# Kernel tuning notes

Hardware: AMD Instinct MI355X
Metric: run time of the kernel (lower is better)

Reference implementation:

```python
import jax, jax.numpy as jnp
import numpy as np


def setup_inputs() -> dict:
    key = jax.random.key(0)
    k1, k2, k3, k4 = jax.random.split(key, 4)
    B, S, D = 2, 2048, 1024
    return {
        "X": jax.random.normal(k1, (B, S, D), dtype=jnp.float32),
        "W_q": jax.random.normal(k2, (D, D), dtype=jnp.float32),
        "W_k": jax.random.normal(k3, (D, D), dtype=jnp.float32),
        "W_v": jax.random.normal(k4, (D, D), dtype=jnp.float32),
        "n_heads": 16,
    }


def reference(X, W_q, W_k, W_v, n_heads):
    B, S, D = X.shape
    H = n_heads
    dh = D // H
    # QKV projections, split heads: [B,S,D] -> [H,B,S,dh]
    def split_heads(Y):
        return Y.reshape(B, S, H, dh).transpose(2, 0, 1, 3)
    Q = split_heads(X @ W_q)
    K = split_heads(X @ W_k)
    V = split_heads(X @ W_v)
    scale = 1.0 / jnp.sqrt(jnp.asarray(dh, dtype=X.dtype))
    # [H,B,S,S] attention scores (naive, matches the original)
    scores = jax.nn.softmax(jnp.einsum("hbqd,hbkd->hbqk", Q, K) * scale, axis=-1)
    out = jnp.einsum("hbqk,hbkd->hbqd", scores, V)  # [H,B,S,dh]
    # torch.concat(out, 0) over leading H dim -> [H*B, S, dh]
    return out.reshape(H * B, S, dh)
```

## Files before the change

### kernel.cpp

```cpp
#include <hip/hip_runtime.h>

typedef unsigned short u16;
typedef unsigned int u32;
typedef __bf16 bf16x8 __attribute__((ext_vector_type(8)));
typedef float f32x4 __attribute__((ext_vector_type(4)));
typedef float f32x16 __attribute__((ext_vector_type(16)));

extern "C" __device__ float __ocml_native_exp2_f32(float);

#define WT_HI_E  ((size_t)0)
#define WT_LO_E  ((size_t)3 << 20)
#define Q_HI_E   ((size_t)14 << 20)
#define Q_LO_E   ((size_t)18 << 20)
#define K_HI_E   ((size_t)22 << 20)
#define K_LO_E   ((size_t)26 << 20)
#define V_HI_E   ((size_t)30 << 20)

__device__ __forceinline__ u16 bf16_rne(float x) {
  u32 u = __float_as_uint(x);
  u32 r = (u + 0x7fffu + ((u >> 16) & 1u)) >> 16;
  return (u16)r;
}
__device__ __forceinline__ float bf16_f(u16 h) {
  return __uint_as_float(((u32)h) << 16);
}
__device__ __forceinline__ u16 f2bf(float x) {
  __bf16 b = (__bf16)x;
  return __builtin_bit_cast(u16, b);
}

__device__ __forceinline__ void gload16(const u16* g, u16* l) {
  __builtin_amdgcn_global_load_lds(
      (const __attribute__((address_space(1))) void*)g,
      (__attribute__((address_space(3))) void*)l, 16, 0, 0);
}

__global__ __launch_bounds__(256) void k_split(const float* __restrict__ w0,
                                               const float* __restrict__ w1,
                                               const float* __restrict__ w2,
                                               u16* __restrict__ ws) {
  int wb = blockIdx.x;
  int z = wb >> 8;
  int rem = wb & 255;
  int by = (rem >> 4) * 64, bx = (rem & 15) * 64;
  const float* W = (z == 0) ? w0 : ((z == 1) ? w1 : w2);
  u16* th = ws + WT_HI_E + (size_t)z * (1u << 20);
  u16* tl = ws + WT_LO_E + (size_t)z * (1u << 20);
  __shared__ float tile[64][65];
  int tx = threadIdx.x & 15, ty = threadIdx.x >> 4;
#pragma unroll
  for (int i = 0; i < 4; i++) {
    int r = ty + i * 16;
    float4 v = *(const float4*)(W + (size_t)(by + r) * 1024 + bx + tx * 4);
    tile[r][tx * 4 + 0] = v.x;
    tile[r][tx * 4 + 1] = v.y;
    tile[r][tx * 4 + 2] = v.z;
    tile[r][tx * 4 + 3] = v.w;
  }
  __syncthreads();
#pragma unroll
  for (int p = 0; p < 2; p++) {
    int t = threadIdx.x + 256 * p;
    int kc = t & 7, nl = t >> 3;
    u32 Hh[4], Ll[4];
#pragma unroll
    for (int u = 0; u < 4; u++) {
      float v0 = tile[kc * 8 + 2 * u][nl];
      float v1 = tile[kc * 8 + 2 * u + 1][nl];
      u16 h0 = f2bf(v0);
      u16 h1 = f2bf(v1);
      u16 l0 = f2bf(v0 - bf16_f(h0));
      u16 l1 = f2bf(v1 - bf16_f(h1));
      Hh[u] = (u32)h0 | ((u32)h1 << 16);
      Ll[u] = (u32)l0 | ((u32)l1 << 16);
    }
    size_t o = (size_t)(bx + nl) * 1024 + by + kc * 8;
    *(uint4*)(th + o) = make_uint4(Hh[0], Hh[1], Hh[2], Hh[3]);
    *(uint4*)(tl + o) = make_uint4(Ll[0], Ll[1], Ll[2], Ll[3]);
  }
}

__global__ __launch_bounds__(256, 4) void k_proj(const float* __restrict__ X,
                                                 u16* __restrict__ ws) {
  int id = blockIdx.x;
  int xcd = id & 7;
  int loc = id >> 3;
  int m_loc = loc & 7;
  int rest = loc >> 3;
  int n_blk = rest & 7, z = rest >> 3;
  int M0 = (xcd * 8 + m_loc) * 64;
  int N0 = n_blk * 128;

  const u16* Wh = ws + WT_HI_E + (size_t)z * (1u << 20);
  const u16* Wl = ws + WT_LO_E + (size_t)z * (1u << 20);
  u16* dsth = ws + ((z == 0) ? Q_HI_E : ((z == 1) ? K_HI_E : V_HI_E));
  u16* dstl = (z == 0) ? (ws + Q_LO_E) : ((z == 1) ? (ws + K_LO_E) : (u16*)0);

  __shared__ u16 smem[12288];
  float* sXf = (float*)smem;
  u16* sWh = smem + 4096;
  u16* sWl = smem + 8192;

  int tid = threadIdx.x, lane = tid & 63, w = tid >> 6;
  int quad = lane >> 4, l16 = lane & 15;
  int mb = (w & 1) * 32, nb = (w >> 1) * 64;

  const f32x4 z4 = {0.f, 0.f, 0.f, 0.f};
  f32x4 acc[4][2];
#pragma unroll
  for (int j = 0; j < 4; j++)
#pragma unroll
    for (int i = 0; i < 2; i++) acc[j][i] = z4;

  for (int kk = 0; kk < 1024; kk += 32) {
    __syncthreads();
    {
#pragma unroll
      for (int j = 0; j < 2; j++) {
        int c = tid + 256 * j;
        int row = c >> 3, q = c & 7;
        int gq = q ^ (row & 7);
        const float* src = X + (size_t)(M0 + row) * 1024 + kk + gq * 4;
        gload16((const u16*)src, &smem[(size_t)(w * 64 + 256 * j) * 8]);
      }
#pragma unroll
      for (int j = 0; j < 2; j++) {
        int c = tid + 256 * j;
        int row = c >> 2, q = c & 3;
        int gq = q ^ ((row >> 1) & 3);
        size_t gw = (size_t)(N0 + row) * 1024 + kk + gq * 8;
        gload16(Wh + gw, &sWh[(size_t)(w * 64 + 256 * j) * 8]);
        if (z != 2) gload16(Wl + gw, &sWl[(size_t)(w * 64 + 256 * j) * 8]);
      }
    }
    __syncthreads();

    bf16x8 bh[4];
#pragma unroll
    for (int j = 0; j < 4; j++) {
      int row = nb + j * 16 + l16;
      bh[j] = *(const bf16x8*)&sWh[row * 32 + (quad ^ ((row >> 1) & 3)) * 8];
    }
    bf16x8 ah[2], al[2];
#pragma unroll
    for (int i = 0; i < 2; i++) {
      int row = mb + i * 16 + l16;
      const float* rp = sXf + row * 32;
      int r7 = row & 7;
      f32x4 xa = *(const f32x4*)(rp + ((quad * 2) ^ r7) * 4);
      f32x4 xb = *(const f32x4*)(rp + ((quad * 2 + 1) ^ r7) * 4);
      bf16x8 hv, lv;
#pragma unroll
      for (int e = 0; e < 4; e++) {
        __bf16 h0 = (__bf16)xa[e];
        hv[e] = h0;
        lv[e] = (__bf16)(xa[e] - (float)h0);
        __bf16 h1 = (__bf16)xb[e];
        hv[4 + e] = h1;
        lv[4 + e] = (__bf16)(xb[e] - (float)h1);
      }
      ah[i] = hv;
      al[i] = lv;
    }

    if (z != 2) {
      bf16x8 bl[4];
#pragma unroll
      for (int j = 0; j < 4; j++) {
        int row = nb + j * 16 + l16;
        bl[j] = *(const bf16x8*)&sWl[row * 32 + (quad ^ ((row >> 1) & 3)) * 8];
      }
#pragma unroll
      for (int j = 0; j < 4; j++)
#pragma unroll
        for (int i = 0; i < 2; i++) {
          f32x4 c0 = acc[j][i];
          c0 = __builtin_amdgcn_mfma_f32_16x16x32_bf16(bh[j], ah[i], c0, 0, 0, 0);
          c0 = __builtin_amdgcn_mfma_f32_16x16x32_bf16(bh[j], al[i], c0, 0, 0, 0);
          c0 = __builtin_amdgcn_mfma_f32_16x16x32_bf16(bl[j], ah[i], c0, 0, 0, 0);
          acc[j][i] = c0;
        }
    } else {
#pragma unroll
      for (int j = 0; j < 4; j++)
#pragma unroll
        for (int i = 0; i < 2; i++)
          acc[j][i] = __builtin_amdgcn_mfma_f32_16x16x32_bf16(ah[i], bh[j], acc[j][i], 0, 0, 0);
    }
  }

  __syncthreads();
  int b = M0 >> 11, S0 = M0 & 2047;

  if (z != 2) {
    u16* my = smem + (size_t)w * 2048;
    int hh = (N0 + nb) >> 6;
    int sbase = S0 + mb;
    float qscale = (z == 0) ? (0.125f * 1.4426950408889634f) : 1.0f;
#pragma unroll
    for (int pass = 0; pass < 2; pass++) {
      u16* dst = pass ? dstl : dsth;
#pragma unroll
      for (int j = 0; j < 4; j++)
#pragma unroll
        for (int i = 0; i < 2; i++) {
          int dl = j * 16 + quad * 4;
          int sl = i * 16 + l16;
          u16 e[4];
#pragma unroll
          for (int r = 0; r < 4; r++) {
            float y = acc[j][i][r] * qscale;
            u16 hv = bf16_rne(y);
            e[r] = pass ? bf16_rne(y - bf16_f(hv)) : hv;
          }
          int elem = sl * 64 + (((dl >> 3) ^ (sl & 7)) << 3) + (dl & 7);
          *(uint2*)&my[elem] = make_uint2((u32)e[0] | ((u32)e[1] << 16),
                                          (u32)e[2] | ((u32)e[3] << 16));
        }
#pragma unroll
      for (int t = 0; t < 4; t++) {
        int sr = (lane >> 3) + t * 8;
        int p = lane & 7;
        int rc = (z == 1) ? p : (p ^ (sr & 7));
        uint4 v = *(const uint4*)&my[sr * 64 + rc * 8];
        size_t o = ((size_t)(hh * 2 + b) * 2048 + sbase + sr) * 64 + p * 8;
        *(uint4*)&dst[o] = v;
      }
    }
  } else {
#pragma unroll
    for (int j = 0; j < 4; j++)
#pragma unroll
      for (int i = 0; i < 2; i++) {
        int dl = j * 16 + l16;
        int s64 = mb + i * 16 + quad * 4;
        u16 e[4];
#pragma unroll
        for (int r = 0; r < 4; r++) e[r] = bf16_rne(acc[j][i][r]);
        int cp = ((s64 >> 3) & 7) ^ (dl & 7);
        int elem = (w >> 1) * 4096 + dl * 64 + (cp << 3) + (s64 & 7);
        *(uint2*)&smem[elem] = make_uint2((u32)e[0] | ((u32)e[1] << 16),
                                          (u32)e[2] | ((u32)e[3] << 16));
      }
    __syncthreads();
    int half = w >> 1;
    int hh = (N0 + half * 64) >> 6;
#pragma unroll
    for (int t = 0; t < 4; t++) {
      int dr = (w & 1) * 32 + (lane >> 3) + t * 8;
      int p = lane & 7;
      uint4 v = *(const uint4*)&smem[half * 4096 + dr * 64 + p * 8];
      size_t o = ((size_t)(hh * 2 + b) * 64 + dr) * 2048 + S0 + p * 8;
      *(uint4*)&dsth[o] = v;
    }
  }
}

__global__ __launch_bounds__(256, 2) void k_attn(u16* __restrict__ ws,
                                                 float* __restrict__ out) {
  const u16* Qh = ws + Q_HI_E;
  const u16* Ql = ws + Q_LO_E;
  const u16* Kh = ws + K_HI_E;
  const u16* Kl = ws + K_LO_E;
  const u16* Vt = ws + V_HI_E;

  __shared__ u16 sKh[2][64][64], sKl[2][64][64], sVt[2][64][64];

  int id = blockIdx.x;
  int hb = id & 31, qb = id >> 5;
  int tid = threadIdx.x, w = tid >> 6, lane = tid & 63;
  int l31 = lane & 31, h = lane >> 5;
  size_t base = (size_t)hb * (2048 * 64);
  int qw0 = qb * 128 + w * 32;

  int srow = lane >> 3, sch = lane & 7;

  auto stage = [&](int buf, int t) {
#pragma unroll
    for (int b2 = 0; b2 < 2; b2++) {
      int rr = w * 16 + b2 * 8;
      size_t kg = base + (size_t)(t * 64 + rr + srow) * 64 + sch * 8;
      gload16(Kh + kg, &sKh[buf][rr][0]);
      gload16(Kl + kg, &sKl[buf][rr][0]);
      size_t vg = base + (size_t)(rr + srow) * 2048 + t * 64 + sch * 8;
      gload16(Vt + vg, &sVt[buf][rr][0]);
    }
  };

  stage(0, 0);

  bf16x8 qh[4], ql[4];
#pragma unroll
  for (int ks = 0; ks < 4; ks++) {
    size_t off = base + (size_t)(qw0 + l31) * 64 + ks * 16 + h * 8;
    qh[ks] = *(const bf16x8*)(Qh + off);
    ql[ks] = *(const bf16x8*)(Ql + off);
  }

  f32x16 o[2];
#pragma unroll
  for (int i = 0; i < 16; i++) { o[0][i] = 0.f; o[1][i] = 0.f; }
  float mr = -1e30f, lr = 0.f;

  auto rdA = [&](const u16 t[64][64], int mt, int ks) -> bf16x8 {
    int ch = ((ks * 2 + h) ^ (l31 & 7)) * 8;
    return *(const bf16x8*)&t[mt * 32 + l31][ch];
  };

  for (int it = 0; it < 32; it++) {
    __syncthreads();
    if (it + 1 < 32) stage((it + 1) & 1, it + 1);
    int buf = it & 1;

    f32x16 sc[2];
#pragma unroll
    for (int i = 0; i < 16; i++) { sc[0][i] = 0.f; sc[1][i] = 0.f; }
#pragma unroll
    for (int ks = 0; ks < 4; ks++)
#pragma unroll
      for (int mt = 0; mt < 2; mt++) {
        bf16x8 kh = rdA(sKh[buf], mt, ks);
        bf16x8 kl = rdA(sKl[buf], mt, ks);
        sc[mt] = __builtin_amdgcn_mfma_f32_32x32x16_bf16(kh, qh[ks], sc[mt], 0, 0, 0);
        sc[mt] = __builtin_amdgcn_mfma_f32_32x32x16_bf16(kh, ql[ks], sc[mt], 0, 0, 0);
        sc[mt] = __builtin_amdgcn_mfma_f32_32x32x16_bf16(kl, qh[ks], sc[mt], 0, 0, 0);
      }

    float mx = sc[0][0];
#pragma unroll
    for (int i = 0; i < 16; i++) {
      mx = fmaxf(mx, sc[0][i]);
      mx = fmaxf(mx, sc[1][i]);
    }
    mx = fmaxf(mx, __shfl_xor(mx, 32));
    float mnew = fmaxf(mr, mx);
    float alpha = __ocml_native_exp2_f32(mr - mnew);
    mr = mnew;
    float rs = 0.f;
    u32 pk[2][8];
#pragma unroll
    for (int t = 0; t < 2; t++)
#pragma unroll
      for (int i = 0; i < 8; i++) {
        float p0 = __ocml_native_exp2_f32(sc[t][2 * i] - mnew);
        float p1 = __ocml_native_exp2_f32(sc[t][2 * i + 1] - mnew);
        rs += p0 + p1;
        u32 a = __float_as_uint(p0) + 0x8000u;
        u32 b = __float_as_uint(p1) + 0x8000u;
        pk[t][i] = __builtin_amdgcn_perm(b, a, 0x07060302u);
      }
    rs += __shfl_xor(rs, 32);
    lr = lr * alpha + rs;
#pragma unroll
    for (int i = 0; i < 16; i++) {
      o[0][i] *= alpha;
      o[1][i] *= alpha;
    }

#pragma unroll
    for (int ks = 0; ks < 4; ks++) {
      int t = ks >> 1, c = ks & 1;
      u32 b0 = pk[t][c * 4 + 0], b1 = pk[t][c * 4 + 1];
      u32 b2 = pk[t][c * 4 + 2], b3 = pk[t][c * 4 + 3];
      u32 rA = (u32)__shfl_xor((int)(h ? b0 : b2), 32);
      u32 rB = (u32)__shfl_xor((int)(h ? b1 : b3), 32);
      uint4 fb = h ? make_uint4(rA, rB, b2, b3) : make_uint4(b0, b1, rA, rB);
      bf16x8 pfrag = *(bf16x8*)&fb;
#pragma unroll
      for (int mt = 0; mt < 2; mt++) {
        bf16x8 vb = rdA(sVt[buf], mt, ks);
        o[mt] = __builtin_amdgcn_mfma_f32_32x32x16_bf16(vb, pfrag, o[mt], 0, 0, 0);
      }
    }
  }

  float inv = 1.f / lr;
  size_t grow = (size_t)hb * 2048 + qw0 + l31;
#pragma unroll
  for (int mt = 0; mt < 2; mt++)
#pragma unroll
    for (int g2 = 0; g2 < 4; g2++) {
      int d0 = mt * 32 + g2 * 8 + 4 * h;
      float4 v = make_float4(o[mt][g2 * 4 + 0] * inv, o[mt][g2 * 4 + 1] * inv,
                             o[mt][g2 * 4 + 2] * inv, o[mt][g2 * 4 + 3] * inv);
      *(float4*)(out + grow * 64 + d0) = v;
    }
}

extern "C" void kernel_launch(void* const* d_in, const int* in_sizes, int n_in,
                              void* d_out, int out_size, void* d_ws, size_t ws_size,
                              hipStream_t stream) {
  const float* X = (const float*)d_in[0];
  const float* Wq = (const float*)d_in[1];
  const float* Wk = (const float*)d_in[2];
  const float* Wv = (const float*)d_in[3];
  u16* ws = (u16*)d_ws;
  float* out = (float*)d_out;

  k_split<<<dim3(768), dim3(256), 0, stream>>>(Wq, Wk, Wv, ws);
  k_proj<<<dim3(1536), dim3(256), 0, stream>>>(X, ws);
  k_attn<<<dim3(512), dim3(256), 0, stream>>>(ws, out);
}
```

Baseline: 226.3 us.

## Add lazy softmax rescaling, MFMA priority hints, and skip lo-split for V projection

In the attention loop, the running-max update and the rescaling of the output accumulator are skipped unless some lane's new max exceeds the old one by more than 8 (log2 domain). This removes per-tile exp and multiply work, at the cost of letting exponentials grow up to 2^8 before renormalising. s_setprio raises wave priority around the MFMA blocks so matrix work is favoured when waves are interleaved. In the projection kernel, the V path (z==2) now converts only the high bf16 part and no longer computes the unused low part.

New measurement: 231.0 us. +2.1%, slower.

```diff
diff --git a/kernel.cpp b/kernel.cpp
--- a/kernel.cpp
+++ b/kernel.cpp
@@ -141,29 +141,33 @@
       int row = nb + j * 16 + l16;
       bh[j] = *(const bf16x8*)&sWh[row * 32 + (quad ^ ((row >> 1) & 3)) * 8];
     }
-    bf16x8 ah[2], al[2];
+    f32x4 xa[2], xb[2];
 #pragma unroll
     for (int i = 0; i < 2; i++) {
       int row = mb + i * 16 + l16;
       const float* rp = sXf + row * 32;
       int r7 = row & 7;
-      f32x4 xa = *(const f32x4*)(rp + ((quad * 2) ^ r7) * 4);
-      f32x4 xb = *(const f32x4*)(rp + ((quad * 2 + 1) ^ r7) * 4);
-      bf16x8 hv, lv;
-#pragma unroll
-      for (int e = 0; e < 4; e++) {
-        __bf16 h0 = (__bf16)xa[e];
-        hv[e] = h0;
-        lv[e] = (__bf16)(xa[e] - (float)h0);
-        __bf16 h1 = (__bf16)xb[e];
-        hv[4 + e] = h1;
-        lv[4 + e] = (__bf16)(xb[e] - (float)h1);
-      }
-      ah[i] = hv;
-      al[i] = lv;
+      xa[i] = *(const f32x4*)(rp + ((quad * 2) ^ r7) * 4);
+      xb[i] = *(const f32x4*)(rp + ((quad * 2 + 1) ^ r7) * 4);
     }
 
     if (z != 2) {
+      bf16x8 ah[2], al[2];
+#pragma unroll
+      for (int i = 0; i < 2; i++) {
+        bf16x8 hv, lv;
+#pragma unroll
+        for (int e = 0; e < 4; e++) {
+          __bf16 h0 = (__bf16)xa[i][e];
+          hv[e] = h0;
+          lv[e] = (__bf16)(xa[i][e] - (float)h0);
+          __bf16 h1 = (__bf16)xb[i][e];
+          hv[4 + e] = h1;
+          lv[4 + e] = (__bf16)(xb[i][e] - (float)h1);
+        }
+        ah[i] = hv;
+        al[i] = lv;
+      }
       bf16x8 bl[4];
 #pragma unroll
       for (int j = 0; j < 4; j++) {
@@ -181,6 +185,17 @@
           acc[j][i] = c0;
         }
     } else {
+      bf16x8 ah[2];
+#pragma unroll
+      for (int i = 0; i < 2; i++) {
+        bf16x8 hv;
+#pragma unroll
+        for (int e = 0; e < 4; e++) {
+          hv[e] = (__bf16)xa[i][e];
+          hv[4 + e] = (__bf16)xb[i][e];
+        }
+        ah[i] = hv;
+      }
 #pragma unroll
       for (int j = 0; j < 4; j++)
 #pragma unroll
@@ -315,6 +330,7 @@
     f32x16 sc[2];
 #pragma unroll
     for (int i = 0; i < 16; i++) { sc[0][i] = 0.f; sc[1][i] = 0.f; }
+    __builtin_amdgcn_s_setprio(1);
 #pragma unroll
     for (int ks = 0; ks < 4; ks++)
 #pragma unroll
@@ -325,6 +341,7 @@
         sc[mt] = __builtin_amdgcn_mfma_f32_32x32x16_bf16(kh, ql[ks], sc[mt], 0, 0, 0);
         sc[mt] = __builtin_amdgcn_mfma_f32_32x32x16_bf16(kl, qh[ks], sc[mt], 0, 0, 0);
       }
+    __builtin_amdgcn_s_setprio(0);
 
     float mx = sc[0][0];
 #pragma unroll
@@ -333,30 +350,34 @@
       mx = fmaxf(mx, sc[1][i]);
     }
     mx = fmaxf(mx, __shfl_xor(mx, 32));
-    float mnew = fmaxf(mr, mx);
-    float alpha = __ocml_native_exp2_f32(mr - mnew);
-    mr = mnew;
+    if (!__all(mx - mr <= 8.0f)) {
+      float mnew = fmaxf(mr, mx);
+      float alpha = __ocml_native_exp2_f32(mr - mnew);
+      mr = mnew;
+      lr *= alpha;
+#pragma unroll
+      for (int i = 0; i < 16; i++) {
+        o[0][i] *= alpha;
+        o[1][i] *= alpha;
+      }
+    }
     float rs = 0.f;
     u32 pk[2][8];
 #pragma unroll
     for (int t = 0; t < 2; t++)
 #pragma unroll
       for (int i = 0; i < 8; i++) {
-        float p0 = __ocml_native_exp2_f32(sc[t][2 * i] - mnew);
-        float p1 = __ocml_native_exp2_f32(sc[t][2 * i + 1] - mnew);
+        float p0 = __ocml_native_exp2_f32(sc[t][2 * i] - mr);
+        float p1 = __ocml_native_exp2_f32(sc[t][2 * i + 1] - mr);
         rs += p0 + p1;
         u32 a = __float_as_uint(p0) + 0x8000u;
         u32 b = __float_as_uint(p1) + 0x8000u;
         pk[t][i] = __builtin_amdgcn_perm(b, a, 0x07060302u);
       }
     rs += __shfl_xor(rs, 32);
-    lr = lr * alpha + rs;
-#pragma unroll
-    for (int i = 0; i < 16; i++) {
-      o[0][i] *= alpha;
-      o[1][i] *= alpha;
-    }
-
+    lr += rs;
+
+    __builtin_amdgcn_s_setprio(1);
 #pragma unroll
     for (int ks = 0; ks < 4; ks++) {
       int t = ks >> 1, c = ks & 1;
@@ -372,6 +393,7 @@
         o[mt] = __builtin_amdgcn_mfma_f32_32x32x16_bf16(vb, pfrag, o[mt], 0, 0, 0);
       }
     }
+    __builtin_amdgcn_s_setprio(0);
   }
 
   float inv = 1.f / lr;
```
